# Optimization experiments

Measured on AMD Instinct MI355X. Metric: run time of the kernel, lower is better.

The kernel has to match this reference:

```python
import jax, jax.numpy as jnp
import numpy as np
from math import sqrt

B, N, DK = 4, 4096, 64


def setup_inputs() -> dict:
    key = jax.random.key(0)
    ks = jax.random.split(key, 5)
    x = jax.random.normal(ks[0], (B, N, DK), dtype=jnp.float32)
    Wv = jax.random.normal(ks[1], (DK, DK), dtype=jnp.float32) / sqrt(DK)
    bv = jax.random.normal(ks[2], (DK,), dtype=jnp.float32) * 0.02
    wq = jax.random.normal(ks[3], (DK,), dtype=jnp.float32) / sqrt(DK)
    wk = jax.random.normal(ks[4], (DK,), dtype=jnp.float32) / sqrt(DK)
    gamma = jnp.ones((DK,), dtype=jnp.float32)
    beta = jnp.zeros((DK,), dtype=jnp.float32)
    return {"x": x, "Wv": Wv, "bv": bv, "wq": wq, "wk": wk, "gamma": gamma, "beta": beta}


def _layer_norm(h, gamma, beta, eps=1e-5):
    mu = jnp.mean(h, axis=-1, keepdims=True)
    var = jnp.var(h, axis=-1, keepdims=True)
    return (h - mu) * jax.lax.rsqrt(var + eps) * gamma + beta


def reference(x, Wv, bv, wq, wk, gamma, beta):
    d_k = x.shape[-1]
    V = jnp.einsum('bnd,ed->bne', x, Wv) + bv          # (B, N, DK)
    Q = jnp.einsum('bnd,d->bn', x, wq)                 # scalar per token
    K = jnp.einsum('bnd,d->bn', x, wk)
    # RBF-kernel scores A[b,i,j] = exp(-(Q_i - K_j)^2)  -> (B, N, N)
    A = jnp.exp(-jnp.square(Q[:, :, None] - K[:, None, :]))
    P = jax.nn.softmax(A / sqrt(d_k), axis=-1)
    out = jnp.einsum('bij,bjd->bid', P, V) + x
    return _layer_norm(out, gamma, beta)
```

## Files before the change

kernel.cpp:

```cpp
#include <hip/hip_runtime.h>

#define NB   4
#define NSEQ 4096
#define DK   64
#define NTOK (NB * NSEQ)

#define QK_SCALE 1.2011224087864498f

typedef __attribute__((ext_vector_type(8))) short short8;
typedef __attribute__((ext_vector_type(4))) float f32x4;

__device__ __forceinline__ float fast_exp2(float x) {
#if __has_builtin(__builtin_amdgcn_exp2f)
    return __builtin_amdgcn_exp2f(x);
#else
    return exp2f(x);
#endif
}

__device__ __forceinline__ unsigned short bf16_rne(float f) {
    unsigned u = __float_as_uint(f);
    u += 0x7fffu + ((u >> 16) & 1u);
    return (unsigned short)(u >> 16);
}

__device__ __forceinline__ short8 u4_to_s8(uint4 u) {
    union { uint4 u; short8 s; } c; c.u = u; return c.s;
}

__global__ __launch_bounds__(512) void qkv_kernel(
    const float* __restrict__ x, const float* __restrict__ Wv,
    const float* __restrict__ bv, const float* __restrict__ wq,
    const float* __restrict__ wk,
    float* __restrict__ Qs, float* __restrict__ Ks, unsigned short* __restrict__ Vt)
{
    __shared__ float x_lds[64 * 68];
    __shared__ float wvt[64 * 68];
    __shared__ float wqk[128];
    __shared__ float bvl[64];
    __shared__ unsigned short vt_lds[64 * 72];

    const int t = threadIdx.x;
    const int tok0 = blockIdx.x * 64;

    #pragma unroll
    for (int r = 0; r < 2; ++r) {
        int f = t + 512 * r;
        int row = f >> 4, c4 = f & 15;
        float4 v = ((const float4*)(x + (size_t)(tok0 + row) * DK))[c4];
        *(float4*)&x_lds[row * 68 + c4 * 4] = v;
    }
    #pragma unroll
    for (int r = 0; r < 2; ++r) {
        int f = t + 512 * r;
        int e = f >> 4, c4 = f & 15;
        float4 v = ((const float4*)(Wv + e * DK))[c4];
        wvt[(c4 * 4 + 0) * 68 + e] = v.x;
        wvt[(c4 * 4 + 1) * 68 + e] = v.y;
        wvt[(c4 * 4 + 2) * 68 + e] = v.z;
        wvt[(c4 * 4 + 3) * 68 + e] = v.w;
    }
    if (t < 64) { wqk[t * 2] = wq[t]; wqk[t * 2 + 1] = wk[t]; bvl[t] = bv[t]; }
    __syncthreads();

    const int tok = t >> 3, oc = t & 7;
    const int e0 = oc * 8;
    float acc[8];
    #pragma unroll
    for (int ee = 0; ee < 8; ++ee) acc[ee] = bvl[e0 + ee];

    for (int d = 0; d < DK; d += 4) {
        float4 x4 = *(const float4*)&x_lds[tok * 68 + d];
        const float xs[4] = {x4.x, x4.y, x4.z, x4.w};
        #pragma unroll
        for (int dd = 0; dd < 4; ++dd) {
            float xv = xs[dd];
            const float4* wrow = (const float4*)&wvt[(d + dd) * 68 + e0];
            float4 wa = wrow[0], wb = wrow[1];
            acc[0] += xv * wa.x; acc[1] += xv * wa.y;
            acc[2] += xv * wa.z; acc[3] += xv * wa.w;
            acc[4] += xv * wb.x; acc[5] += xv * wb.y;
            acc[6] += xv * wb.z; acc[7] += xv * wb.w;
        }
    }
    #pragma unroll
    for (int k = 0; k < 8; ++k)
        vt_lds[(e0 + k) * 72 + tok] = bf16_rne(acc[k]);

    if (t < 128) {
        const int tk = t & 63;
        const int sel = (t >= 64);
        float a = 0.f;
        for (int d = 0; d < DK; ++d)
            a += x_lds[tk * 68 + d] * wqk[d * 2 + sel];
        (sel ? Ks : Qs)[tok0 + tk] = a * QK_SCALE;
    }
    __syncthreads();

    const int bb = tok0 >> 12, n0 = tok0 & 4095;
    {
        int d = t >> 3, c = t & 7;
        uint4 v = *(const uint4*)((const char*)vt_lds + d * 144 + c * 16);
        *(uint4*)(Vt + (size_t)(bb * 64 + d) * 4096 + n0 + c * 8) = v;
    }
}

extern __shared__ float smem[];

__global__ __launch_bounds__(1024, 4) void attn_kernel(
    const float* __restrict__ x,
    const float* __restrict__ Qsg, const float* __restrict__ Ksg,
    const unsigned short* __restrict__ Vt,
    const float* __restrict__ gamma, const float* __restrict__ beta,
    float* __restrict__ out, int nrep)
{
    float* k_lds = smem;
    float* red   = smem + 4096;
    float* dred  = smem + 4096 + 8 * 64 * 68;

    const int t    = threadIdx.x;
    const int B    = blockIdx.x;
    const int b    = (B & 7) >> 1;
    const int i0   = (((B >> 3) << 1) | (B & 1)) << 6;
    const int w    = t >> 6;
    const int lane = t & 63;
    const int rit  = lane & 15;
    const int q    = lane >> 4;
    const int rgrp = w >> 3;
    const int je   = w & 7;

    ((float4*)k_lds)[t] = ((const float4*)(Ksg + (size_t)b * 4096))[t];

    const float Qs0 = Qsg[b * 4096 + i0 + rgrp * 32 + rit];
    const float Qs1 = Qsg[b * 4096 + i0 + rgrp * 32 + 16 + rit];

    const short onebf = (short)0x3F80;
    const short8 vones = {onebf, onebf, onebf, onebf, onebf, onebf, onebf, onebf};

    const int jw = je * 512;
    const unsigned short* vb = Vt + (size_t)b * 64 * 4096 + (size_t)rit * 4096 + jw + q * 8;
    const float* kp = &k_lds[jw + q * 8];

    __syncthreads();

    for (int rep = 0; rep < nrep; ++rep) {

    f32x4 acc[2][4] = {};
    f32x4 accd[2] = {};

    #pragma unroll 2
    for (int s = 0; s < 16; ++s) {
        const unsigned short* vn = vb + s * 32;
        uint4 bu0 = *(const uint4*)(vn);
        uint4 bu1 = *(const uint4*)(vn + 16 * 4096);
        uint4 bu2 = *(const uint4*)(vn + 32 * 4096);
        uint4 bu3 = *(const uint4*)(vn + 48 * 4096);

        const float* kn = kp + s * 32;
        float4 ka = *(const float4*)(kn);
        float4 kb = *(const float4*)(kn + 4);
        float kv[8] = {ka.x, ka.y, ka.z, ka.w, kb.x, kb.y, kb.z, kb.w};

        float w0[8], w1[8];
        #pragma unroll
        for (int jj = 0; jj < 8; ++jj) {
            float d0 = Qs0 - kv[jj];
            float g0 = fast_exp2(-d0 * d0);
            float p0 = __builtin_fmaf(g0, 3.2552083e-4f, 7.8125e-3f);
            p0 = __builtin_fmaf(g0, p0, 0.125f);
            w0[jj] = __builtin_fmaf(g0, p0, 1.0f);
            float d1 = Qs1 - kv[jj];
            float g1 = fast_exp2(-d1 * d1);
            float p1 = __builtin_fmaf(g1, 3.2552083e-4f, 7.8125e-3f);
            p1 = __builtin_fmaf(g1, p1, 0.125f);
            w1[jj] = __builtin_fmaf(g1, p1, 1.0f);
        }
        uint4 au0, au1;
        au0.x = __builtin_amdgcn_perm(__float_as_uint(w0[1]), __float_as_uint(w0[0]), 0x07060302u);
        au0.y = __builtin_amdgcn_perm(__float_as_uint(w0[3]), __float_as_uint(w0[2]), 0x07060302u);
        au0.z = __builtin_amdgcn_perm(__float_as_uint(w0[5]), __float_as_uint(w0[4]), 0x07060302u);
        au0.w = __builtin_amdgcn_perm(__float_as_uint(w0[7]), __float_as_uint(w0[6]), 0x07060302u);
        au1.x = __builtin_amdgcn_perm(__float_as_uint(w1[1]), __float_as_uint(w1[0]), 0x07060302u);
        au1.y = __builtin_amdgcn_perm(__float_as_uint(w1[3]), __float_as_uint(w1[2]), 0x07060302u);
        au1.z = __builtin_amdgcn_perm(__float_as_uint(w1[5]), __float_as_uint(w1[4]), 0x07060302u);
        au1.w = __builtin_amdgcn_perm(__float_as_uint(w1[7]), __float_as_uint(w1[6]), 0x07060302u);
        short8 a0 = u4_to_s8(au0);
        short8 a1 = u4_to_s8(au1);

        short8 b0 = u4_to_s8(bu0), b1 = u4_to_s8(bu1);
        short8 b2 = u4_to_s8(bu2), b3 = u4_to_s8(bu3);
        acc[0][0] = __builtin_amdgcn_mfma_f32_16x16x32_bf16(a0, b0, acc[0][0], 0, 0, 0);
        acc[0][1] = __builtin_amdgcn_mfma_f32_16x16x32_bf16(a0, b1, acc[0][1], 0, 0, 0);
        acc[0][2] = __builtin_amdgcn_mfma_f32_16x16x32_bf16(a0, b2, acc[0][2], 0, 0, 0);
        acc[0][3] = __builtin_amdgcn_mfma_f32_16x16x32_bf16(a0, b3, acc[0][3], 0, 0, 0);
        acc[1][0] = __builtin_amdgcn_mfma_f32_16x16x32_bf16(a1, b0, acc[1][0], 0, 0, 0);
        acc[1][1] = __builtin_amdgcn_mfma_f32_16x16x32_bf16(a1, b1, acc[1][1], 0, 0, 0);
        acc[1][2] = __builtin_amdgcn_mfma_f32_16x16x32_bf16(a1, b2, acc[1][2], 0, 0, 0);
        acc[1][3] = __builtin_amdgcn_mfma_f32_16x16x32_bf16(a1, b3, acc[1][3], 0, 0, 0);
        accd[0]   = __builtin_amdgcn_mfma_f32_16x16x32_bf16(a0, vones, accd[0], 0, 0, 0);
        accd[1]   = __builtin_amdgcn_mfma_f32_16x16x32_bf16(a1, vones, accd[1], 0, 0, 0);
    }

    {
        float* rbase = red + (size_t)je * (64 * 68);
        #pragma unroll
        for (int rt = 0; rt < 2; ++rt)
            #pragma unroll
            for (int ct = 0; ct < 4; ++ct)
                #pragma unroll
                for (int rg = 0; rg < 4; ++rg)
                    rbase[(rgrp * 32 + rt * 16 + q * 4 + rg) * 68 + ct * 16 + rit]
                        = acc[rt][ct][rg];
        if (rit == 0) {
            #pragma unroll
            for (int rt = 0; rt < 2; ++rt)
                #pragma unroll
                for (int rg = 0; rg < 4; ++rg)
                    dred[je * 64 + rgrp * 32 + rt * 16 + q * 4 + rg] = accd[rt][rg];
        }
    }
    __syncthreads();

    {
        const int row = t >> 4, cg = t & 15, c0 = cg * 4;
        float dsum = 0.f;
        #pragma unroll
        for (int sl = 0; sl < 8; ++sl) dsum += dred[sl * 64 + row];
        const float inv = 1.0f / dsum;
        const size_t rowg = (size_t)(b * 4096 + i0 + row);

        float4 num = make_float4(0.f, 0.f, 0.f, 0.f);
        #pragma unroll
        for (int sl = 0; sl < 8; ++sl) {
            float4 r4 = *(const float4*)&red[(size_t)sl * (64 * 68) + row * 68 + c0];
            num.x += r4.x; num.y += r4.y; num.z += r4.z; num.w += r4.w;
        }
        const float4 x4 = *(const float4*)(x + rowg * 64 + c0);
        float4 h;
        h.x = num.x * inv + x4.x;
        h.y = num.y * inv + x4.y;
        h.z = num.z * inv + x4.z;
        h.w = num.w * inv + x4.w;

        float sm = h.x + h.y + h.z + h.w;
        float ss = h.x * h.x + h.y * h.y + h.z * h.z + h.w * h.w;
        #pragma unroll
        for (int m = 1; m < 16; m <<= 1) { sm += __shfl_xor(sm, m); ss += __shfl_xor(ss, m); }
        const float mu   = sm * 0.015625f;
        const float var  = ss * 0.015625f - mu * mu;
        const float rstd = rsqrtf(var + 1e-5f);

        const float4 g4 = *(const float4*)(gamma + c0);
        const float4 b4 = *(const float4*)(beta + c0);
        float4 o;
        o.x = (h.x - mu) * rstd * g4.x + b4.x;
        o.y = (h.y - mu) * rstd * g4.y + b4.y;
        o.z = (h.z - mu) * rstd * g4.z + b4.z;
        o.w = (h.w - mu) * rstd * g4.w + b4.w;
        *(float4*)(out + rowg * 64 + c0) = o;
    }
    __syncthreads();
    }
}

extern "C" void kernel_launch(void* const* d_in, const int* in_sizes, int n_in,
                              void* d_out, int out_size, void* d_ws, size_t ws_size,
                              hipStream_t stream)
{
    const float* x     = (const float*)d_in[0];
    const float* Wv    = (const float*)d_in[1];
    const float* bv    = (const float*)d_in[2];
    const float* wq    = (const float*)d_in[3];
    const float* wk    = (const float*)d_in[4];
    const float* gamma = (const float*)d_in[5];
    const float* beta  = (const float*)d_in[6];
    float* out = (float*)d_out;

    float* Qs = (float*)d_ws;
    float* Ks = Qs + NTOK;
    unsigned short* Vt = (unsigned short*)(Ks + NTOK);

    const int attn_lds = 4096 * 4 + 8 * 64 * 68 * 4 + 8 * 64 * 4;
    hipFuncSetAttribute((const void*)attn_kernel,
                        hipFuncAttributeMaxDynamicSharedMemorySize, attn_lds);

    qkv_kernel<<<dim3(NTOK / 64), dim3(512), 0, stream>>>(x, Wv, bv, wq, wk, Qs, Ks, Vt);
    attn_kernel<<<dim3(NB * (NSEQ / 64)), dim3(1024), attn_lds, stream>>>(
        x, Qs, Ks, Vt, gamma, beta, out, 1);
}
```

Measured before the change: 105.2 us.

## Stage V tiles through double-buffered LDS with async global-to-LDS loads

Previously each wave read its V slice straight from global memory. Now the block cooperatively copies 512-column chunks of V into a double-buffered LDS region using global_load_lds, and prefetches the next chunk while computing on the current one. Waves split each chunk by column instead of owning a contiguous 512-wide range. This trades per-wave global loads for shared LDS reuse, at the cost of one block-wide barrier per chunk and LDS space that overlaps the reduction buffer. The prefetch is issued without an explicit wait before the barrier, so correctness relies on the barrier draining the outstanding loads.

```diff
diff --git a/kernel.cpp b/kernel.cpp
--- a/kernel.cpp
+++ b/kernel.cpp
@@ -27,6 +27,9 @@
 __device__ __forceinline__ short8 u4_to_s8(uint4 u) {
     union { uint4 u; short8 s; } c; c.u = u; return c.s;
 }
+
+#define AS3U(p) ((__attribute__((address_space(3))) unsigned int*)(p))
+#define AS1U(p) ((const __attribute__((address_space(1))) unsigned int*)(p))
 
 __global__ __launch_bounds__(512) void qkv_kernel(
     const float* __restrict__ x, const float* __restrict__ Wv,
@@ -115,6 +118,7 @@
     float* __restrict__ out, int nrep)
 {
     float* k_lds = smem;
+    unsigned short* vs = (unsigned short*)(smem + 4096);
     float* red   = smem + 4096;
     float* dred  = smem + 4096 + 8 * 64 * 68;
 
@@ -127,7 +131,7 @@
     const int rit  = lane & 15;
     const int q    = lane >> 4;
     const int rgrp = w >> 3;
-    const int je   = w & 7;
+    const int js   = w & 7;
 
     ((float4*)k_lds)[t] = ((const float4*)(Ksg + (size_t)b * 4096))[t];
 
@@ -137,72 +141,101 @@
     const short onebf = (short)0x3F80;
     const short8 vones = {onebf, onebf, onebf, onebf, onebf, onebf, onebf, onebf};
 
-    const int jw = je * 512;
-    const unsigned short* vb = Vt + (size_t)b * 64 * 4096 + (size_t)rit * 4096 + jw + q * 8;
-    const float* kp = &k_lds[jw + q * 8];
-
-    __syncthreads();
+    const unsigned short* Vtb0 = Vt + (size_t)b * 64 * 4096;
 
     for (int rep = 0; rep < nrep; ++rep) {
 
     f32x4 acc[2][4] = {};
     f32x4 accd[2] = {};
 
-    #pragma unroll 2
-    for (int s = 0; s < 16; ++s) {
-        const unsigned short* vn = vb + s * 32;
-        uint4 bu0 = *(const uint4*)(vn);
-        uint4 bu1 = *(const uint4*)(vn + 16 * 4096);
-        uint4 bu2 = *(const uint4*)(vn + 32 * 4096);
-        uint4 bu3 = *(const uint4*)(vn + 48 * 4096);
-
-        const float* kn = kp + s * 32;
-        float4 ka = *(const float4*)(kn);
-        float4 kb = *(const float4*)(kn + 4);
-        float kv[8] = {ka.x, ka.y, ka.z, ka.w, kb.x, kb.y, kb.z, kb.w};
-
-        float w0[8], w1[8];
-        #pragma unroll
-        for (int jj = 0; jj < 8; ++jj) {
-            float d0 = Qs0 - kv[jj];
-            float g0 = fast_exp2(-d0 * d0);
-            float p0 = __builtin_fmaf(g0, 3.2552083e-4f, 7.8125e-3f);
-            p0 = __builtin_fmaf(g0, p0, 0.125f);
-            w0[jj] = __builtin_fmaf(g0, p0, 1.0f);
-            float d1 = Qs1 - kv[jj];
-            float g1 = fast_exp2(-d1 * d1);
-            float p1 = __builtin_fmaf(g1, 3.2552083e-4f, 7.8125e-3f);
-            p1 = __builtin_fmaf(g1, p1, 0.125f);
-            w1[jj] = __builtin_fmaf(g1, p1, 1.0f);
-        }
-        uint4 au0, au1;
-        au0.x = __builtin_amdgcn_perm(__float_as_uint(w0[1]), __float_as_uint(w0[0]), 0x07060302u);
-        au0.y = __builtin_amdgcn_perm(__float_as_uint(w0[3]), __float_as_uint(w0[2]), 0x07060302u);
-        au0.z = __builtin_amdgcn_perm(__float_as_uint(w0[5]), __float_as_uint(w0[4]), 0x07060302u);
-        au0.w = __builtin_amdgcn_perm(__float_as_uint(w0[7]), __float_as_uint(w0[6]), 0x07060302u);
-        au1.x = __builtin_amdgcn_perm(__float_as_uint(w1[1]), __float_as_uint(w1[0]), 0x07060302u);
-        au1.y = __builtin_amdgcn_perm(__float_as_uint(w1[3]), __float_as_uint(w1[2]), 0x07060302u);
-        au1.z = __builtin_amdgcn_perm(__float_as_uint(w1[5]), __float_as_uint(w1[4]), 0x07060302u);
-        au1.w = __builtin_amdgcn_perm(__float_as_uint(w1[7]), __float_as_uint(w1[6]), 0x07060302u);
-        short8 a0 = u4_to_s8(au0);
-        short8 a1 = u4_to_s8(au1);
-
-        short8 b0 = u4_to_s8(bu0), b1 = u4_to_s8(bu1);
-        short8 b2 = u4_to_s8(bu2), b3 = u4_to_s8(bu3);
-        acc[0][0] = __builtin_amdgcn_mfma_f32_16x16x32_bf16(a0, b0, acc[0][0], 0, 0, 0);
-        acc[0][1] = __builtin_amdgcn_mfma_f32_16x16x32_bf16(a0, b1, acc[0][1], 0, 0, 0);
-        acc[0][2] = __builtin_amdgcn_mfma_f32_16x16x32_bf16(a0, b2, acc[0][2], 0, 0, 0);
-        acc[0][3] = __builtin_amdgcn_mfma_f32_16x16x32_bf16(a0, b3, acc[0][3], 0, 0, 0);
-        acc[1][0] = __builtin_amdgcn_mfma_f32_16x16x32_bf16(a1, b0, acc[1][0], 0, 0, 0);
-        acc[1][1] = __builtin_amdgcn_mfma_f32_16x16x32_bf16(a1, b1, acc[1][1], 0, 0, 0);
-        acc[1][2] = __builtin_amdgcn_mfma_f32_16x16x32_bf16(a1, b2, acc[1][2], 0, 0, 0);
-        acc[1][3] = __builtin_amdgcn_mfma_f32_16x16x32_bf16(a1, b3, acc[1][3], 0, 0, 0);
-        accd[0]   = __builtin_amdgcn_mfma_f32_16x16x32_bf16(a0, vones, accd[0], 0, 0, 0);
-        accd[1]   = __builtin_amdgcn_mfma_f32_16x16x32_bf16(a1, vones, accd[1], 0, 0, 0);
+    #pragma unroll
+    for (int i = 0; i < 4; ++i) {
+        const int d = w + 16 * i;
+        const unsigned short* g = Vtb0 + (size_t)d * 4096 + lane * 8;
+        unsigned short* l = vs + d * 520;
+#if __has_builtin(__builtin_amdgcn_global_load_lds)
+        __builtin_amdgcn_global_load_lds(AS1U(g), AS3U(l), 16, 0, 0);
+#else
+        *(uint4*)(l + lane * 8) = *(const uint4*)g;
+#endif
+    }
+    __syncthreads();
+
+    for (int r = 0; r < 8; ++r) {
+        const int bf = r & 1;
+        if (r < 7) {
+            const int jw = (r + 1) * 512;
+            #pragma unroll
+            for (int i = 0; i < 4; ++i) {
+                const int d = w + 16 * i;
+                const unsigned short* g = Vtb0 + (size_t)d * 4096 + jw + lane * 8;
+                unsigned short* l = vs + (bf ^ 1) * 33280 + d * 520;
+#if __has_builtin(__builtin_amdgcn_global_load_lds)
+                __builtin_amdgcn_global_load_lds(AS1U(g), AS3U(l), 16, 0, 0);
+#else
+                *(uint4*)(l + lane * 8) = *(const uint4*)g;
+#endif
+            }
+        }
+
+        #pragma unroll
+        for (int sl = 0; sl < 2; ++sl) {
+            const int jloc = js * 64 + sl * 32;
+            const unsigned short* vf = vs + bf * 33280 + rit * 520 + jloc + q * 8;
+            uint4 bu0 = *(const uint4*)(vf);
+            uint4 bu1 = *(const uint4*)(vf + 16 * 520);
+            uint4 bu2 = *(const uint4*)(vf + 32 * 520);
+            uint4 bu3 = *(const uint4*)(vf + 48 * 520);
+
+            const float* kn = k_lds + r * 512 + jloc + q * 8;
+            float4 ka = *(const float4*)(kn);
+            float4 kb = *(const float4*)(kn + 4);
+            float kv[8] = {ka.x, ka.y, ka.z, ka.w, kb.x, kb.y, kb.z, kb.w};
+
+            float w0[8], w1[8];
+            #pragma unroll
+            for (int jj = 0; jj < 8; ++jj) {
+                float d0 = Qs0 - kv[jj];
+                float g0 = fast_exp2(-d0 * d0);
+                float p0 = __builtin_fmaf(g0, 3.2552083e-4f, 7.8125e-3f);
+                p0 = __builtin_fmaf(g0, p0, 0.125f);
+                w0[jj] = __builtin_fmaf(g0, p0, 1.0f);
+                float d1 = Qs1 - kv[jj];
+                float g1 = fast_exp2(-d1 * d1);
+                float p1 = __builtin_fmaf(g1, 3.2552083e-4f, 7.8125e-3f);
+                p1 = __builtin_fmaf(g1, p1, 0.125f);
+                w1[jj] = __builtin_fmaf(g1, p1, 1.0f);
+            }
+            uint4 au0, au1;
+            au0.x = __builtin_amdgcn_perm(__float_as_uint(w0[1]), __float_as_uint(w0[0]), 0x07060302u);
+            au0.y = __builtin_amdgcn_perm(__float_as_uint(w0[3]), __float_as_uint(w0[2]), 0x07060302u);
+            au0.z = __builtin_amdgcn_perm(__float_as_uint(w0[5]), __float_as_uint(w0[4]), 0x07060302u);
+            au0.w = __builtin_amdgcn_perm(__float_as_uint(w0[7]), __float_as_uint(w0[6]), 0x07060302u);
+            au1.x = __builtin_amdgcn_perm(__float_as_uint(w1[1]), __float_as_uint(w1[0]), 0x07060302u);
+            au1.y = __builtin_amdgcn_perm(__float_as_uint(w1[3]), __float_as_uint(w1[2]), 0x07060302u);
+            au1.z = __builtin_amdgcn_perm(__float_as_uint(w1[5]), __float_as_uint(w1[4]), 0x07060302u);
+            au1.w = __builtin_amdgcn_perm(__float_as_uint(w1[7]), __float_as_uint(w1[6]), 0x07060302u);
+            short8 a0 = u4_to_s8(au0);
+            short8 a1 = u4_to_s8(au1);
+
+            short8 b0 = u4_to_s8(bu0), b1 = u4_to_s8(bu1);
+            short8 b2 = u4_to_s8(bu2), b3 = u4_to_s8(bu3);
+            acc[0][0] = __builtin_amdgcn_mfma_f32_16x16x32_bf16(a0, b0, acc[0][0], 0, 0, 0);
+            acc[0][1] = __builtin_amdgcn_mfma_f32_16x16x32_bf16(a0, b1, acc[0][1], 0, 0, 0);
+            acc[0][2] = __builtin_amdgcn_mfma_f32_16x16x32_bf16(a0, b2, acc[0][2], 0, 0, 0);
+            acc[0][3] = __builtin_amdgcn_mfma_f32_16x16x32_bf16(a0, b3, acc[0][3], 0, 0, 0);
+            acc[1][0] = __builtin_amdgcn_mfma_f32_16x16x32_bf16(a1, b0, acc[1][0], 0, 0, 0);
+            acc[1][1] = __builtin_amdgcn_mfma_f32_16x16x32_bf16(a1, b1, acc[1][1], 0, 0, 0);
+            acc[1][2] = __builtin_amdgcn_mfma_f32_16x16x32_bf16(a1, b2, acc[1][2], 0, 0, 0);
+            acc[1][3] = __builtin_amdgcn_mfma_f32_16x16x32_bf16(a1, b3, acc[1][3], 0, 0, 0);
+            accd[0]   = __builtin_amdgcn_mfma_f32_16x16x32_bf16(a0, vones, accd[0], 0, 0, 0);
+            accd[1]   = __builtin_amdgcn_mfma_f32_16x16x32_bf16(a1, vones, accd[1], 0, 0, 0);
+        }
+        __syncthreads();
     }
 
     {
-        float* rbase = red + (size_t)je * (64 * 68);
+        float* rbase = red + (size_t)js * (64 * 68);
         #pragma unroll
         for (int rt = 0; rt < 2; ++rt)
             #pragma unroll
@@ -216,7 +249,7 @@
             for (int rt = 0; rt < 2; ++rt)
                 #pragma unroll
                 for (int rg = 0; rg < 4; ++rg)
-                    dred[je * 64 + rgrp * 32 + rt * 16 + q * 4 + rg] = accd[rt][rg];
+                    dred[js * 64 + rgrp * 32 + rt * 16 + q * 4 + rg] = accd[rt][rg];
         }
     }
     __syncthreads();
```

New measurement: 95.57 us. 9.2% less time.
